# Performance work log

Hardware: AMD Instinct MI355X
Metric: run time of the kernel (lower is better)

The kernel has to match this reference:

```python
import jax, jax.numpy as jnp
import numpy as np

N_NODES = 50000
N_EDGES = 800000
MUL = 32            # multiplicity of 0e and 1o feature irreps
N_SPECIES = 4       # node_attr = 4x0e one-hot
N_BASIS = 8         # radial basis scalars
N_HID = 8           # invariant_neurons
AVG_NEIGH = 16.0
INV_SQRT3 = 1.0 / np.sqrt(3.0).astype(np.float32)


def setup_inputs() -> dict:
    key = jax.random.key(0)
    ks = jax.random.split(key, 16)
    x = jax.random.normal(ks[0], (N_NODES, MUL * 4), jnp.float32)  # 32x0e + 32x1o
    species = jax.random.randint(ks[1], (N_NODES,), 0, N_SPECIES)
    node_attr = jax.nn.one_hot(species, N_SPECIES, dtype=jnp.float32)
    edge_embedding = jax.random.normal(ks[2], (N_EDGES, N_BASIS), jnp.float32)
    edge_attr = jax.random.normal(ks[3], (N_EDGES, 4), jnp.float32)  # 1x0e + 1x1o
    edge_index = jax.random.randint(ks[4], (2, N_EDGES), 0, N_NODES)
    # learned params
    W_lin1_s = jax.random.normal(ks[5], (MUL, MUL), jnp.float32)
    W_lin1_v = jax.random.normal(ks[6], (MUL, MUL), jnp.float32)
    fc_w1 = jax.random.normal(ks[7], (N_BASIS, N_HID), jnp.float32)
    fc_w2 = jax.random.normal(ks[8], (N_HID, 4 * MUL), jnp.float32)  # tp.weight_numel = 4*MUL
    W_lin2_s = jax.random.normal(ks[9], (2 * MUL, MUL), jnp.float32)  # mid simplify: 64x0e
    W_lin2_v = jax.random.normal(ks[10], (2 * MUL, MUL), jnp.float32)  # 64x1o
    W_sc_s = jax.random.normal(ks[11], (MUL, N_SPECIES, MUL), jnp.float32)
    W_sc_v = jax.random.normal(ks[12], (MUL, N_SPECIES, MUL), jnp.float32)
    return dict(node_features=x, node_attr=node_attr, edge_embedding=edge_embedding,
                edge_attr=edge_attr, edge_index=edge_index,
                W_lin1_s=W_lin1_s, W_lin1_v=W_lin1_v, fc_w1=fc_w1, fc_w2=fc_w2,
                W_lin2_s=W_lin2_s, W_lin2_v=W_lin2_v, W_sc_s=W_sc_s, W_sc_v=W_sc_v)


def _forward(node_features, node_attr, edge_embedding, edge_attr, edge_index,
             W_lin1_s, W_lin1_v, fc_w1, fc_w2, W_lin2_s, W_lin2_v, W_sc_s, W_sc_v):
    n = node_features.shape[0]
    xs = node_features[:, :MUL]                       # [N, 32] scalars (0e)
    xv = node_features[:, MUL:].reshape(n, MUL, 3)    # [N, 32, 3] vectors (1o)

    # self-connection: FullyConnectedTensorProduct(feat, 4x0e -> feat), uvw weights
    sc_norm = 1.0 / np.sqrt(MUL * N_SPECIES).astype(np.float32)
    sc_s = jnp.einsum('nu,nv,uvw->nw', xs, node_attr, W_sc_s) * sc_norm
    sc_v = jnp.einsum('nui,nv,uvw->nwi', xv, node_attr, W_sc_v) * sc_norm

    # linear_1: per-irrep channel mixing, 1/sqrt(fan_in)
    l1n = 1.0 / np.sqrt(MUL).astype(np.float32)
    ys = (xs @ W_lin1_s) * l1n
    yv = jnp.einsum('nui,uw->nwi', xv, W_lin1_v) * l1n

    # radial MLP -> per-edge tensor-product weights (4 paths x MUL)
    h = jax.nn.silu((edge_embedding @ fc_w1) / np.sqrt(N_BASIS).astype(np.float32))
    w = (h @ fc_w2) / np.sqrt(N_HID).astype(np.float32)  # [E, 128]
    w00, w01, w10, w11 = jnp.split(w, 4, axis=1)          # instruction order (0,0),(0,1),(1,0),(1,1)

    src = edge_index[0]
    dst = edge_index[1]
    es = ys[src]                                          # [E, 32]
    ev = yv[src]                                          # [E, 32, 3]
    a0 = edge_attr[:, 0]                                  # [E]    0e
    a1 = edge_attr[:, 1:4]                                # [E, 3] 1o

    # per-edge weighted uvu tensor product paths
    o_s_a = w00 * es * a0[:, None]                                       # 0e x 0e -> 0e
    o_s_b = w11 * jnp.einsum('eui,ei->eu', ev, a1) * INV_SQRT3           # 1o x 1o -> 0e
    o_v_a = (w01 * es)[:, :, None] * a1[:, None, :]                      # 0e x 1o -> 1o
    o_v_b = w10[:, :, None] * ev * a0[:, None, None]                     # 1o x 0e -> 1o

    # scatter-sum to destination nodes
    mid_s = jax.ops.segment_sum(jnp.concatenate([o_s_a, o_s_b], axis=1), dst, num_segments=n)
    mid_v = jax.ops.segment_sum(jnp.concatenate([o_v_a, o_v_b], axis=1), dst, num_segments=n)
    inv = 1.0 / np.sqrt(AVG_NEIGH).astype(np.float32)
    mid_s = mid_s * inv   # [N, 64]
    mid_v = mid_v * inv   # [N, 64, 3]

    # linear_2: 64x0e+64x1o -> 32x0e+32x1o
    l2n = 1.0 / np.sqrt(2 * MUL).astype(np.float32)
    out_s = (mid_s @ W_lin2_s) * l2n + sc_s
    out_v = jnp.einsum('nui,uw->nwi', mid_v, W_lin2_v) * l2n + sc_v
    return jnp.concatenate([out_s, out_v.reshape(n, MUL * 3)], axis=1)


def reference(node_features, node_attr, edge_embedding, edge_attr, edge_index,
              W_lin1_s, W_lin1_v, fc_w1, fc_w2, W_lin2_s, W_lin2_v, W_sc_s, W_sc_v):
    return _forward(node_features, node_attr, edge_embedding, edge_attr, edge_index,
                    W_lin1_s, W_lin1_v, fc_w1, fc_w2, W_lin2_s, W_lin2_v, W_sc_s, W_sc_v)
```

## Files before the change

### kernel.cpp

```cpp
#include <hip/hip_runtime.h>
#include <hip/hip_bf16.h>

#define N_NODES 50000
#define N_EDGES 800000
#define CAP 64
#define NODE_BLOCKS 1250
#define BUCKET_BLOCKS (N_EDGES/256)

__device__ __forceinline__ unsigned short f2bf(float f) {
    union { float f; unsigned u; } t; t.f = f;
    unsigned r = t.u + 0x7FFF + ((t.u >> 16) & 1);
    return (unsigned short)(r >> 16);
}

__global__ __launch_bounds__(256) void prep_kernel(
    const float* __restrict__ x, const float* __restrict__ attr,
    const float* __restrict__ W1s, const float* __restrict__ W1v,
    const float* __restrict__ Wscs, const float* __restrict__ Wscv,
    const int* __restrict__ eidx,
    int* __restrict__ counts, int* __restrict__ bucket,
    unsigned short* __restrict__ ysvh, float* __restrict__ out)
{
    __shared__ float shm[9216];
    const int tid = threadIdx.x;

    if (blockIdx.x < NODE_BLOCKS) {
        const int nl = tid >> 5;
        const int w  = tid & 31;

        float w1s[32], w1v[32];
        #pragma unroll
        for (int u = 0; u < 32; ++u) {
            w1s[u] = W1s[u*32 + w];
            w1v[u] = W1v[u*32 + w];
        }
        #pragma unroll
        for (int i = 0; i < 4; ++i) {
            ((float4*)(shm + 1024))[tid + i*256] = ((const float4*)Wscs)[tid + i*256];
            ((float4*)(shm + 5120))[tid + i*256] = ((const float4*)Wscv)[tid + i*256];
        }

        const float l1n = 0.17677669529663687f;
        const float scn = 0.08838834764831843f;

        for (int batch = 0; batch < 5; ++batch) {
            const int node0 = blockIdx.x * 40 + batch * 8;
            __syncthreads();
            ((float4*)shm)[tid] = ((const float4*)(x + (long)node0 * 128))[tid];
            __syncthreads();

            const int node = node0 + nl;
            const float* at = attr + (long)node * 4;
            int sp = 0;
            if (at[1] > 0.5f) sp = 1;
            if (at[2] > 0.5f) sp = 2;
            if (at[3] > 0.5f) sp = 3;

            const float* lx   = shm + nl * 128;
            const float* lscs = shm + 1024 + sp * 32;
            const float* lscv = shm + 5120 + sp * 32;

            float ys = 0.f, yv0 = 0.f, yv1 = 0.f, yv2 = 0.f;
            float ss = 0.f, sv0 = 0.f, sv1 = 0.f, sv2 = 0.f;
            #pragma unroll
            for (int u4 = 0; u4 < 8; ++u4) {
                const float4 xs4 = ((const float4*)lx)[u4];
                const float4 q0  = ((const float4*)(lx + 32))[u4*3 + 0];
                const float4 q1  = ((const float4*)(lx + 32))[u4*3 + 1];
                const float4 q2  = ((const float4*)(lx + 32))[u4*3 + 2];
                const float xsv[4]  = {xs4.x, xs4.y, xs4.z, xs4.w};
                const float xvv[12] = {q0.x,q0.y,q0.z,q0.w,
                                       q1.x,q1.y,q1.z,q1.w,
                                       q2.x,q2.y,q2.z,q2.w};
                #pragma unroll
                for (int j = 0; j < 4; ++j) {
                    const int u = u4*4 + j;
                    const float wss = lscs[u*128 + w];
                    const float wsv = lscv[u*128 + w];
                    ys  += xsv[j] * w1s[u];
                    yv0 += xvv[3*j+0] * w1v[u];
                    yv1 += xvv[3*j+1] * w1v[u];
                    yv2 += xvv[3*j+2] * w1v[u];
                    ss  += xsv[j] * wss;
                    sv0 += xvv[3*j+0] * wsv;
                    sv1 += xvv[3*j+1] * wsv;
                    sv2 += xvv[3*j+2] * wsv;
                }
            }

            uint2 pk;
            pk.x = (unsigned)f2bf(ys  * l1n) | ((unsigned)f2bf(yv0 * l1n) << 16);
            pk.y = (unsigned)f2bf(yv1 * l1n) | ((unsigned)f2bf(yv2 * l1n) << 16);
            *(uint2*)(ysvh + (long)node * 128 + w * 4) = pk;

            float* op = out + (long)node * 128;
            op[w] = ss * scn;
            op[32 + 3*w + 0] = sv0 * scn;
            op[32 + 3*w + 1] = sv1 * scn;
            op[32 + 3*w + 2] = sv2 * scn;
        }
    } else {
        const int e = (blockIdx.x - NODE_BLOCKS) * 256 + tid;
        const int dst = eidx[N_EDGES + e];
        const int slot = atomicAdd(&counts[dst], 1);
        if (slot < CAP) bucket[(long)dst * CAP + slot] = e;
    }
}

__global__ __launch_bounds__(256) void agg_kernel(
    const float* __restrict__ ee, const float* __restrict__ eattr,
    const int* __restrict__ eidx,
    const float* __restrict__ fcw1, const float* __restrict__ fcw2,
    const float* __restrict__ W2s, const float* __restrict__ W2v,
    const unsigned short* __restrict__ ysvh,
    const int* __restrict__ counts, const int* __restrict__ bucket,
    float* __restrict__ out)
{
    __shared__ float hrec[8][32 * 12];

    const int tid = threadIdx.x;
    const int nl = tid >> 5;
    const int u  = tid & 31;
    const int node = blockIdx.x * 8 + nl;
    const float inv_sqrt8 = 0.35355339059327373f;

    float f2r[8][4];
    #pragma unroll
    for (int j = 0; j < 8; ++j) {
        f2r[j][0] = fcw2[j*128 + u];
        f2r[j][1] = fcw2[j*128 + 32 + u];
        f2r[j][2] = fcw2[j*128 + 64 + u];
        f2r[j][3] = fcw2[j*128 + 96 + u];
    }

    const int cnt = min(counts[node], CAP);
    int e0 = bucket[(long)node * CAP + u];
    const bool dummy = (u >= cnt);
    if (dummy) e0 = 0;
    const int s0 = dummy ? 0 : eidx[e0];

    {
        const float4 ea = ((const float4*)(ee + (long)e0 * 8))[0];
        const float4 eb = ((const float4*)(ee + (long)e0 * 8))[1];
        const float4 at = ((const float4*)eattr)[e0];
        const float eev[8] = {ea.x, ea.y, ea.z, ea.w, eb.x, eb.y, eb.z, eb.w};
        float* hr = hrec[nl] + u * 12;
        float h[8];
        #pragma unroll
        for (int j = 0; j < 8; ++j) {
            float pre = 0.f;
            #pragma unroll
            for (int b = 0; b < 8; ++b) pre += eev[b] * fcw1[b*8 + j];
            pre *= inv_sqrt8;
            const float s = pre / (1.f + __expf(-pre)) * inv_sqrt8;
            h[j] = dummy ? 0.f : s;
        }
        ((float4*)hr)[0] = make_float4(h[0], h[1], h[2], h[3]);
        ((float4*)hr)[1] = make_float4(h[4], h[5], h[6], h[7]);
        ((float4*)hr)[2] = at;
    }

    float msa = 0.f, msb = 0.f;
    float va0 = 0.f, va1 = 0.f, va2 = 0.f;
    float vb0 = 0.f, vb1 = 0.f, vb2 = 0.f;

    #define ACCUM(HA, HB, AT, Y)                                             \
    {                                                                        \
        const float es = __uint_as_float((Y).x << 16);                       \
        const float ex = __uint_as_float((Y).x & 0xffff0000u);               \
        const float ey = __uint_as_float((Y).y << 16);                       \
        const float ez = __uint_as_float((Y).y & 0xffff0000u);               \
        const float hh[8] = {HA.x,HA.y,HA.z,HA.w,HB.x,HB.y,HB.z,HB.w};       \
        float w00=0.f, w01=0.f, w10=0.f, w11=0.f;                            \
        _Pragma("unroll")                                                    \
        for (int j = 0; j < 8; ++j) {                                        \
            w00 += hh[j]*f2r[j][0]; w01 += hh[j]*f2r[j][1];                  \
            w10 += hh[j]*f2r[j][2]; w11 += hh[j]*f2r[j][3];                  \
        }                                                                    \
        const float a0 = AT.x, a1x = AT.y, a1y = AT.z, a1z = AT.w;           \
        msa += w00 * es * a0;                                                \
        msb += w11 * (ex*a1x + ey*a1y + ez*a1z);                             \
        const float t = w01 * es;                                            \
        va0 += t*a1x; va1 += t*a1y; va2 += t*a1z;                            \
        const float s = w10 * a0;                                            \
        vb0 += s*ex; vb1 += s*ey; vb2 += s*ez;                               \
    }

    #define GATHER(SLOT) \
        (*(const uint2*)(ysvh + (long)__shfl(s0, (SLOT), 32) * 128 + u * 4))

    const int c0 = min(cnt, 32);
    {
        uint2 y0 = GATHER(0), y1 = GATHER(1), y2 = GATHER(2), y3 = GATHER(3);
        for (int k = 0; k < c0; k += 4) {
            const int kn = (k + 4) & 31;
            const uint2 n0 = GATHER(kn);
            const uint2 n1 = GATHER(kn + 1);
            const uint2 n2 = GATHER(kn + 2);
            const uint2 n3 = GATHER(kn + 3);
            const float4* h0p = (const float4*)(hrec[nl] + (k + 0) * 12);
            const float4* h1p = (const float4*)(hrec[nl] + (k + 1) * 12);
            const float4* h2p = (const float4*)(hrec[nl] + (k + 2) * 12);
            const float4* h3p = (const float4*)(hrec[nl] + (k + 3) * 12);
            const float4 A0 = h0p[0], B0 = h0p[1], T0 = h0p[2];
            const float4 A1 = h1p[0], B1 = h1p[1], T1 = h1p[2];
            const float4 A2 = h2p[0], B2 = h2p[1], T2 = h2p[2];
            const float4 A3 = h3p[0], B3 = h3p[1], T3 = h3p[2];
            ACCUM(A0, B0, T0, y0)
            ACCUM(A1, B1, T1, y1)
            ACCUM(A2, B2, T2, y2)
            ACCUM(A3, B3, T3, y3)
            y0 = n0; y1 = n1; y2 = n2; y3 = n3;
        }
    }

    if (cnt > 32) {
        int be = bucket[(long)node * CAP + min(32 + u, CAP-1)];
        if (32 + u >= cnt) be = 0;
        for (int k = 32; k < cnt; ++k) {
            const int e = __shfl(be, k - 32, 32);
            const int s = eidx[e];
            const float4 ea = ((const float4*)(ee + (long)e * 8))[0];
            const float4 eb = ((const float4*)(ee + (long)e * 8))[1];
            const float4 at = ((const float4*)eattr)[e];
            const float eev[8] = {ea.x, ea.y, ea.z, ea.w, eb.x, eb.y, eb.z, eb.w};
            float h[8];
            #pragma unroll
            for (int j = 0; j < 8; ++j) {
                float pre = 0.f;
                #pragma unroll
                for (int b = 0; b < 8; ++b) pre += eev[b] * fcw1[b*8 + j];
                pre *= inv_sqrt8;
                h[j] = pre / (1.f + __expf(-pre)) * inv_sqrt8;
            }
            const float4 HA = make_float4(h[0], h[1], h[2], h[3]);
            const float4 HB = make_float4(h[4], h[5], h[6], h[7]);
            const uint2 y = *(const uint2*)(ysvh + (long)s * 128 + u * 4);
            ACCUM(HA, HB, at, y)
        }
    }
    #undef GATHER
    #undef ACCUM

    msb *= 0.5773502691896258f;

    float* m = hrec[nl];
    m[u]       = msa;
    m[32 + u]  = msb;
    m[64  + u*3 + 0] = va0;  m[64  + u*3 + 1] = va1;  m[64  + u*3 + 2] = va2;
    m[160 + u*3 + 0] = vb0;  m[160 + u*3 + 1] = vb1;  m[160 + u*3 + 2] = vb2;

    float os = 0.f, ov0 = 0.f, ov1 = 0.f, ov2 = 0.f;
    #pragma unroll 8
    for (int q = 0; q < 32; ++q) {
        const float wsa = W2s[q*32 + u];
        const float wsb = W2s[(32 + q)*32 + u];
        os += m[q] * wsa + m[32 + q] * wsb;
        const float wva = W2v[q*32 + u];
        const float wvb = W2v[(32 + q)*32 + u];
        ov0 += m[64 + q*3 + 0] * wva + m[160 + q*3 + 0] * wvb;
        ov1 += m[64 + q*3 + 1] * wva + m[160 + q*3 + 1] * wvb;
        ov2 += m[64 + q*3 + 2] * wva + m[160 + q*3 + 2] * wvb;
    }

    const float sc = 0.03125f;
    float* op = out + (long)node * 128;
    op[u]            += os  * sc;
    op[32 + 3*u + 0] += ov0 * sc;
    op[32 + 3*u + 1] += ov1 * sc;
    op[32 + 3*u + 2] += ov2 * sc;
}

extern "C" void kernel_launch(void* const* d_in, const int* in_sizes, int n_in,
                              void* d_out, int out_size, void* d_ws, size_t ws_size,
                              hipStream_t stream) {
    const float* x     = (const float*)d_in[0];
    const float* attr  = (const float*)d_in[1];
    const float* ee    = (const float*)d_in[2];
    const float* eattr = (const float*)d_in[3];
    const int*   eidx  = (const int*)  d_in[4];
    const float* W1s   = (const float*)d_in[5];
    const float* W1v   = (const float*)d_in[6];
    const float* fcw1  = (const float*)d_in[7];
    const float* fcw2  = (const float*)d_in[8];
    const float* W2s   = (const float*)d_in[9];
    const float* W2v   = (const float*)d_in[10];
    const float* Wscs  = (const float*)d_in[11];
    const float* Wscv  = (const float*)d_in[12];

    float* out = (float*)d_out;

    unsigned short* ysvh = (unsigned short*)d_ws;
    int*   counts = (int*)(ysvh + (long)N_NODES * 128);
    int*   bucket = counts + N_NODES;

    hipMemsetAsync(counts, 0, N_NODES * sizeof(int), stream);
    prep_kernel<<<NODE_BLOCKS + BUCKET_BLOCKS, 256, 0, stream>>>(
        x, attr, W1s, W1v, Wscs, Wscv, eidx, counts, bucket, ysvh, out);
    agg_kernel<<<N_NODES/8, 256, 0, stream>>>(ee, eattr, eidx, fcw1, fcw2,
                                              W2s, W2v, ysvh, counts, bucket, out);
}
```

Baseline: 299.0 us.

## Precompute per-edge radial MLP payload in prep kernel for coalesced agg reads

The edge-bucketing blocks of the prep kernel now also compute the radial MLP hidden values for each edge. They pack those values, the edge attributes and the source index into a 64-byte record in workspace. The aggregation kernel then reads one contiguous record per edge instead of gathering from eidx, ee and eattr and recomputing the MLP. This removes scattered reads and repeated SiLU math from the agg kernel, at the cost of about 51 MB of extra writes and reads through workspace. The path is taken only when the workspace is large enough, and the second-stage LDS buffer is split into a separate array.

```diff
diff --git a/kernel.cpp b/kernel.cpp
--- a/kernel.cpp
+++ b/kernel.cpp
@@ -13,12 +13,16 @@
     return (unsigned short)(r >> 16);
 }
 
+template<bool EP>
 __global__ __launch_bounds__(256) void prep_kernel(
     const float* __restrict__ x, const float* __restrict__ attr,
     const float* __restrict__ W1s, const float* __restrict__ W1v,
     const float* __restrict__ Wscs, const float* __restrict__ Wscv,
+    const float* __restrict__ ee, const float* __restrict__ eattr,
+    const float* __restrict__ fcw1,
     const int* __restrict__ eidx,
     int* __restrict__ counts, int* __restrict__ bucket,
+    float* __restrict__ epay,
     unsigned short* __restrict__ ysvh, float* __restrict__ out)
 {
     __shared__ float shm[9216];
@@ -102,11 +106,34 @@
     } else {
         const int e = (blockIdx.x - NODE_BLOCKS) * 256 + tid;
         const int dst = eidx[N_EDGES + e];
+        if (EP) {
+            const float inv_sqrt8 = 0.35355339059327373f;
+            const int src = eidx[e];
+            const float4 ea = ((const float4*)(ee + (long)e * 8))[0];
+            const float4 eb = ((const float4*)(ee + (long)e * 8))[1];
+            const float4 at = ((const float4*)eattr)[e];
+            const float eev[8] = {ea.x, ea.y, ea.z, ea.w, eb.x, eb.y, eb.z, eb.w};
+            float h[8];
+            #pragma unroll
+            for (int j = 0; j < 8; ++j) {
+                float pre = 0.f;
+                #pragma unroll
+                for (int b = 0; b < 8; ++b) pre += eev[b] * fcw1[b*8 + j];
+                pre *= inv_sqrt8;
+                h[j] = pre / (1.f + __expf(-pre)) * inv_sqrt8;
+            }
+            float4* ep = (float4*)(epay + (long)e * 16);
+            ep[0] = make_float4(h[0], h[1], h[2], h[3]);
+            ep[1] = make_float4(h[4], h[5], h[6], h[7]);
+            ep[2] = at;
+            ep[3] = make_float4(__int_as_float(src), 0.f, 0.f, 0.f);
+        }
         const int slot = atomicAdd(&counts[dst], 1);
         if (slot < CAP) bucket[(long)dst * CAP + slot] = e;
     }
 }
 
+template<bool EP>
 __global__ __launch_bounds__(256) void agg_kernel(
     const float* __restrict__ ee, const float* __restrict__ eattr,
     const int* __restrict__ eidx,
@@ -114,9 +141,11 @@
     const float* __restrict__ W2s, const float* __restrict__ W2v,
     const unsigned short* __restrict__ ysvh,
     const int* __restrict__ counts, const int* __restrict__ bucket,
+    const float* __restrict__ epay,
     float* __restrict__ out)
 {
     __shared__ float hrec[8][32 * 12];
+    __shared__ float mid[8][256];
 
     const int tid = threadIdx.x;
     const int nl = tid >> 5;
@@ -137,9 +166,23 @@
     int e0 = bucket[(long)node * CAP + u];
     const bool dummy = (u >= cnt);
     if (dummy) e0 = 0;
-    const int s0 = dummy ? 0 : eidx[e0];
-
-    {
+    int s0;
+
+    if (EP) {
+        const float4* ep = (const float4*)(epay + (long)e0 * 16);
+        float4 p0 = ep[0], p1 = ep[1];
+        const float4 p2 = ep[2], p3 = ep[3];
+        s0 = dummy ? 0 : __float_as_int(p3.x);
+        if (dummy) {
+            p0 = make_float4(0.f, 0.f, 0.f, 0.f);
+            p1 = make_float4(0.f, 0.f, 0.f, 0.f);
+        }
+        float* hr = hrec[nl] + u * 12;
+        ((float4*)hr)[0] = p0;
+        ((float4*)hr)[1] = p1;
+        ((float4*)hr)[2] = p2;
+    } else {
+        s0 = dummy ? 0 : eidx[e0];
         const float4 ea = ((const float4*)(ee + (long)e0 * 8))[0];
         const float4 eb = ((const float4*)(ee + (long)e0 * 8))[1];
         const float4 at = ((const float4*)eattr)[e0];
@@ -215,28 +258,36 @@
     }
 
     if (cnt > 32) {
-        int be = bucket[(long)node * CAP + min(32 + u, CAP-1)];
+        int be = bucket[(long)node * CAP + 32 + u];
         if (32 + u >= cnt) be = 0;
         for (int k = 32; k < cnt; ++k) {
             const int e = __shfl(be, k - 32, 32);
-            const int s = eidx[e];
-            const float4 ea = ((const float4*)(ee + (long)e * 8))[0];
-            const float4 eb = ((const float4*)(ee + (long)e * 8))[1];
-            const float4 at = ((const float4*)eattr)[e];
-            const float eev[8] = {ea.x, ea.y, ea.z, ea.w, eb.x, eb.y, eb.z, eb.w};
-            float h[8];
-            #pragma unroll
-            for (int j = 0; j < 8; ++j) {
-                float pre = 0.f;
+            if (EP) {
+                const float4* ep = (const float4*)(epay + (long)e * 16);
+                const float4 HA = ep[0], HB = ep[1], at = ep[2];
+                const int s = __float_as_int(ep[3].x);
+                const uint2 y = *(const uint2*)(ysvh + (long)s * 128 + u * 4);
+                ACCUM(HA, HB, at, y)
+            } else {
+                const int s = eidx[e];
+                const float4 ea = ((const float4*)(ee + (long)e * 8))[0];
+                const float4 eb = ((const float4*)(ee + (long)e * 8))[1];
+                const float4 at = ((const float4*)eattr)[e];
+                const float eev[8] = {ea.x, ea.y, ea.z, ea.w, eb.x, eb.y, eb.z, eb.w};
+                float h[8];
                 #pragma unroll
-                for (int b = 0; b < 8; ++b) pre += eev[b] * fcw1[b*8 + j];
-                pre *= inv_sqrt8;
-                h[j] = pre / (1.f + __expf(-pre)) * inv_sqrt8;
+                for (int j = 0; j < 8; ++j) {
+                    float pre = 0.f;
+                    #pragma unroll
+                    for (int b = 0; b < 8; ++b) pre += eev[b] * fcw1[b*8 + j];
+                    pre *= inv_sqrt8;
+                    h[j] = pre / (1.f + __expf(-pre)) * inv_sqrt8;
+                }
+                const float4 HA = make_float4(h[0], h[1], h[2], h[3]);
+                const float4 HB = make_float4(h[4], h[5], h[6], h[7]);
+                const uint2 y = *(const uint2*)(ysvh + (long)s * 128 + u * 4);
+                ACCUM(HA, HB, at, y)
             }
-            const float4 HA = make_float4(h[0], h[1], h[2], h[3]);
-            const float4 HB = make_float4(h[4], h[5], h[6], h[7]);
-            const uint2 y = *(const uint2*)(ysvh + (long)s * 128 + u * 4);
-            ACCUM(HA, HB, at, y)
         }
     }
     #undef GATHER
@@ -244,7 +295,7 @@
 
     msb *= 0.5773502691896258f;
 
-    float* m = hrec[nl];
+    float* m = mid[nl];
     m[u]       = msa;
     m[32 + u]  = msb;
     m[64  + u*3 + 0] = va0;  m[64  + u*3 + 1] = va1;  m[64  + u*3 + 2] = va2;
@@ -293,10 +344,23 @@
     unsigned short* ysvh = (unsigned short*)d_ws;
     int*   counts = (int*)(ysvh + (long)N_NODES * 128);
     int*   bucket = counts + N_NODES;
+    float* epay   = (float*)(bucket + (long)N_NODES * CAP);
+
+    const size_t need = (size_t)N_NODES*256 + (size_t)N_NODES*4
+                      + (size_t)N_NODES*CAP*4 + (size_t)N_EDGES*64;
 
     hipMemsetAsync(counts, 0, N_NODES * sizeof(int), stream);
-    prep_kernel<<<NODE_BLOCKS + BUCKET_BLOCKS, 256, 0, stream>>>(
-        x, attr, W1s, W1v, Wscs, Wscv, eidx, counts, bucket, ysvh, out);
-    agg_kernel<<<N_NODES/8, 256, 0, stream>>>(ee, eattr, eidx, fcw1, fcw2,
-                                              W2s, W2v, ysvh, counts, bucket, out);
+    if (ws_size >= need) {
+        prep_kernel<true><<<NODE_BLOCKS + BUCKET_BLOCKS, 256, 0, stream>>>(
+            x, attr, W1s, W1v, Wscs, Wscv, ee, eattr, fcw1, eidx,
+            counts, bucket, epay, ysvh, out);
+        agg_kernel<true><<<N_NODES/8, 256, 0, stream>>>(ee, eattr, eidx, fcw1, fcw2,
+            W2s, W2v, ysvh, counts, bucket, epay, out);
+    } else {
+        prep_kernel<false><<<NODE_BLOCKS + BUCKET_BLOCKS, 256, 0, stream>>>(
+            x, attr, W1s, W1v, Wscs, Wscv, ee, eattr, fcw1, eidx,
+            counts, bucket, epay, ysvh, out);
+        agg_kernel<false><<<N_NODES/8, 256, 0, stream>>>(ee, eattr, eidx, fcw1, fcw2,
+            W2s, W2v, ysvh, counts, bucket, epay, out);
+    }
 }
```

Result: faster. 275.6 us (-7.8%).
